# Optimization experiments

Measured on AMD Instinct MI355X. Metric: run time of the kernel, lower is better.

## Reference

```python
import jax, jax.numpy as jnp
import numpy as np

DIM = 128       # model dim d
NEXP = 64       # number of experts
K = 2           # top-k (hardcoded in the module)
B, S = 1, 1024  # batch, seq
HID = DIM * 4   # expert FFN hidden = 4*d


def _gelu(v):
    # torch F.gelu / nn.GELU default = exact erf form
    return jax.nn.gelu(v, approximate=False)


def setup_inputs() -> dict:
    key = jax.random.key(0)
    ks = jax.random.split(key, 8)
    sc = 0.02
    xav = (2.0 / (HID + DIM)) ** 0.5  # xavier_normal std for [4d, d]
    x = jax.random.normal(ks[0], (B, S, DIM), jnp.float32)
    # gate MLP: Linear(d,4d) -> GELU -> Linear(4d,4d) -> GELU -> Linear(4d,E) -> Sigmoid
    gw1 = jax.random.normal(ks[1], (DIM, HID), jnp.float32) * sc
    gb1 = jnp.zeros((HID,), jnp.float32)
    gw2 = jax.random.normal(ks[2], (HID, HID), jnp.float32) * sc
    gb2 = jnp.zeros((HID,), jnp.float32)
    gw3 = jax.random.normal(ks[3], (HID, NEXP), jnp.float32) * sc
    gb3 = jnp.zeros((NEXP,), jnp.float32)
    # expert banks (shapes fixed to the consistent 2-layer FFN reading)
    W1 = jax.random.normal(ks[4], (NEXP, HID, DIM), jnp.float32) * xav
    B1 = jnp.zeros((NEXP, HID), jnp.float32)
    W2 = jax.random.normal(ks[5], (NEXP, DIM, HID), jnp.float32) * xav
    B2 = jnp.zeros((NEXP, DIM), jnp.float32)
    return dict(x=x, gw1=gw1, gb1=gb1, gw2=gw2, gb2=gb2, gw3=gw3, gb3=gb3,
                W1=W1, B1=B1, W2=W2, B2=B2)


def reference(x, gw1, gb1, gw2, gb2, gw3, gb3, W1, B1, W2, B2):
    # gating network -> sigmoid scores over experts
    h = _gelu(x @ gw1 + gb1)
    h = _gelu(h @ gw2 + gb2)
    gate = jax.nn.sigmoid(h @ gw3 + gb3)                 # [B,S,E]
    values, idx = jax.lax.top_k(gate, K)                 # [B,S,K]
    values = values / jnp.sum(values, axis=-1, keepdims=True)
    # naive per-token gather of full expert weights (matches original access pattern)
    w1g = W1[idx]                                        # [B,S,K,HID,DIM]
    b1g = B1[idx]                                        # [B,S,K,HID]
    w2g = W2[idx]                                        # [B,S,K,DIM,HID]
    b2g = B2[idx]                                        # [B,S,K,DIM]
    t = _gelu(jnp.einsum('bskfd,bsd->bskf', w1g, x) + b1g)   # [B,S,K,HID]
    y = _gelu(jnp.einsum('bskdf,bskf->bskd', w2g, t) + b2g)  # [B,S,K,DIM]
    return jnp.sum(y * values[..., None], axis=-2)           # [B,S,DIM]
```

## Files before the change

kernel.cpp:

```cpp
#include <hip/hip_runtime.h>
#include <math.h>

#define NDIM 128
#define NHID 512
#define NEXPERT 64
#define NTOK 1024
#define NPAIR (NTOK * 2)

typedef __attribute__((ext_vector_type(8))) short short8_t;
typedef __attribute__((ext_vector_type(4))) float f32x4;

__device__ __forceinline__ float gelu_f(float v) {
    return 0.5f * v * (1.0f + erff(v * 0.7071067811865476f));
}
__device__ __forceinline__ unsigned short f2bf(float f) {
    union { float f; unsigned u; } v; v.f = f;
    unsigned r = v.u + 0x7FFFu + ((v.u >> 16) & 1u);
    return (unsigned short)(r >> 16);
}
__device__ __forceinline__ float bf2f(unsigned short h) {
    union { unsigned u; float f; } v; v.u = ((unsigned)h) << 16;
    return v.f;
}
__device__ __forceinline__ void split3(float f, short& ho, short& mo, short& lo) {
    const unsigned short h = f2bf(f);
    const float r1 = f - bf2f(h);
    const unsigned short m = f2bf(r1);
    const unsigned short l = f2bf(r1 - bf2f(m));
    ho = (short)h; mo = (short)m; lo = (short)l;
}

__global__ __launch_bounds__(256) void k_g1d2(
        const float* __restrict__ x, const float* __restrict__ gw1,
        const float* __restrict__ gw2, const float* __restrict__ gb1,
        unsigned short* __restrict__ G2h, unsigned short* __restrict__ G2m,
        unsigned short* __restrict__ G2l, unsigned short* __restrict__ Hh,
        unsigned short* __restrict__ Hm, unsigned short* __restrict__ Hl) {
    __shared__ __align__(16) char smem[58112];
    const int j = threadIdx.x;
    if (blockIdx.x >= 256) {
        float (*T)[65] = (float (*)[65])smem;
        const int u = blockIdx.x - 256;
        const int k0 = (u >> 3) * 64, n0 = (u & 7) * 64;
#pragma unroll
        for (int q = 0; q < 4; ++q) {
            const int idx = j + 256 * q;
            const int kr = idx >> 4, c4 = idx & 15;
            float4 v = *(const float4*)(gw2 + (size_t)(k0 + kr) * NHID + n0 + c4 * 4);
            T[kr][c4 * 4 + 0] = v.x; T[kr][c4 * 4 + 1] = v.y;
            T[kr][c4 * 4 + 2] = v.z; T[kr][c4 * 4 + 3] = v.w;
        }
        __syncthreads();
#pragma unroll
        for (int q = 0; q < 4; ++q) {
            const int idx = j + 256 * q;
            const int n = idx >> 4, k4 = idx & 15;
            short4 sh, sm, sl;
#pragma unroll
            for (int qq = 0; qq < 4; ++qq)
                split3(T[k4 * 4 + qq][n], (&sh.x)[qq], (&sm.x)[qq], (&sl.x)[qq]);
            const size_t o = (size_t)(n0 + n) * NHID + k0 + k4 * 4;
            *(short4*)(G2h + o) = sh;
            *(short4*)(G2m + o) = sm;
            *(short4*)(G2l + o) = sl;
        }
        return;
    }
    short (*Ahs)[32][72] = (short (*)[32][72])smem;
    short (*Bss)[64][72] = (short (*)[64][72])(smem + 13824);
    float (*T)[65] = (float (*)[65])(smem + 41472);
    const int u = blockIdx.x;
    const int m0 = (u >> 3) * 32, n0 = (u & 7) * 64;
    const int w = j >> 6, lane = j & 63;
    const int mt = w & 1, npair = w >> 1;
    const int lrow = lane & 15, lseg = lane >> 4;
    f32x4 acc[2];
    acc[0] = (f32x4){0.f, 0.f, 0.f, 0.f};
    acc[1] = (f32x4){0.f, 0.f, 0.f, 0.f};
    for (int kc = 0; kc < NDIM; kc += 64) {
        __syncthreads();
#pragma unroll
        for (int q = 0; q < 4; ++q) {
            const int idx = j + 256 * q;
            const int kr = idx >> 4, c4 = idx & 15;
            float4 v = *(const float4*)(gw1 + (size_t)(kc + kr) * NHID + n0 + c4 * 4);
            T[kr][c4 * 4 + 0] = v.x; T[kr][c4 * 4 + 1] = v.y;
            T[kr][c4 * 4 + 2] = v.z; T[kr][c4 * 4 + 3] = v.w;
        }
#pragma unroll
        for (int q = 0; q < 2; ++q) {
            const int idx = j + 256 * q;
            const int row = idx >> 4, c4 = idx & 15;
            float4 v = *(const float4*)(x + (size_t)(m0 + row) * NDIM + kc + c4 * 4);
            short4 sh, sm, sl;
#pragma unroll
            for (int qq = 0; qq < 4; ++qq)
                split3((&v.x)[qq], (&sh.x)[qq], (&sm.x)[qq], (&sl.x)[qq]);
            *(short4*)&Ahs[0][row][c4 * 4] = sh;
            *(short4*)&Ahs[1][row][c4 * 4] = sm;
            *(short4*)&Ahs[2][row][c4 * 4] = sl;
        }
        __syncthreads();
#pragma unroll
        for (int q = 0; q < 4; ++q) {
            const int idx = j + 256 * q;
            const int nn = idx >> 4, k4 = idx & 15;
            short4 sh, sm, sl;
#pragma unroll
            for (int qq = 0; qq < 4; ++qq)
                split3(T[k4 * 4 + qq][nn], (&sh.x)[qq], (&sm.x)[qq], (&sl.x)[qq]);
            *(short4*)&Bss[0][nn][k4 * 4] = sh;
            *(short4*)&Bss[1][nn][k4 * 4] = sm;
            *(short4*)&Bss[2][nn][k4 * 4] = sl;
        }
        __syncthreads();
#pragma unroll
        for (int ks = 0; ks < 2; ++ks) {
            const int ko = ks * 32 + lseg * 8;
            short8_t ah = *(short8_t*)&Ahs[0][mt * 16 + lrow][ko];
            short8_t am = *(short8_t*)&Ahs[1][mt * 16 + lrow][ko];
            short8_t al = *(short8_t*)&Ahs[2][mt * 16 + lrow][ko];
#pragma unroll
            for (int nt = 0; nt < 2; ++nt) {
                const int nr = (npair * 2 + nt) * 16 + lrow;
                short8_t bh = *(short8_t*)&Bss[0][nr][ko];
                short8_t bm = *(short8_t*)&Bss[1][nr][ko];
                short8_t bl = *(short8_t*)&Bss[2][nr][ko];
                acc[nt] = __builtin_amdgcn_mfma_f32_16x16x32_bf16(ah, bh, acc[nt], 0, 0, 0);
                acc[nt] = __builtin_amdgcn_mfma_f32_16x16x32_bf16(am, bh, acc[nt], 0, 0, 0);
                acc[nt] = __builtin_amdgcn_mfma_f32_16x16x32_bf16(ah, bm, acc[nt], 0, 0, 0);
                acc[nt] = __builtin_amdgcn_mfma_f32_16x16x32_bf16(al, bh, acc[nt], 0, 0, 0);
                acc[nt] = __builtin_amdgcn_mfma_f32_16x16x32_bf16(ah, bl, acc[nt], 0, 0, 0);
                acc[nt] = __builtin_amdgcn_mfma_f32_16x16x32_bf16(am, bm, acc[nt], 0, 0, 0);
            }
        }
    }
#pragma unroll
    for (int nt = 0; nt < 2; ++nt) {
        const int col = n0 + (npair * 2 + nt) * 16 + lrow;
        const float bb = gb1[col];
#pragma unroll
        for (int r = 0; r < 4; ++r) {
            const int row = m0 + mt * 16 + lseg * 4 + r;
            const float h = gelu_f(acc[nt][r] + bb);
            short hh, hm, hl;
            split3(h, hh, hm, hl);
            const size_t o = (size_t)row * NHID + col;
            Hh[o] = (unsigned short)hh; Hm[o] = (unsigned short)hm;
            Hl[o] = (unsigned short)hl;
        }
    }
}

__global__ __launch_bounds__(256) void k_gate2(
        const unsigned short* __restrict__ Ahp, const unsigned short* __restrict__ Amp,
        const unsigned short* __restrict__ Alp,
        const unsigned short* __restrict__ Bhp, const unsigned short* __restrict__ Bmp,
        const unsigned short* __restrict__ Blp,
        const float* __restrict__ gb2, float* __restrict__ h2) {
    __shared__ short Ahs[3][32][72];
    __shared__ short Bss[3][64][72];
    const int j = threadIdx.x;
    const int u = blockIdx.x;
    const int m0 = (u >> 3) * 32, n0 = (u & 7) * 64;
    const int w = j >> 6, lane = j & 63;
    const int mt = w & 1, npair = w >> 1;
    const int lrow = lane & 15, lseg = lane >> 4;
    const int K = NHID;
    f32x4 acc[2];
    acc[0] = (f32x4){0.f, 0.f, 0.f, 0.f};
    acc[1] = (f32x4){0.f, 0.f, 0.f, 0.f};
    for (int kc = 0; kc < K; kc += 64) {
        __syncthreads();
        {
            const int row = j >> 3, c8 = j & 7;
            const size_t o = (size_t)(m0 + row) * K + kc + c8 * 8;
            *(short8_t*)&Ahs[0][row][c8 * 8] = *(const short8_t*)(Ahp + o);
            *(short8_t*)&Ahs[1][row][c8 * 8] = *(const short8_t*)(Amp + o);
            *(short8_t*)&Ahs[2][row][c8 * 8] = *(const short8_t*)(Alp + o);
        }
#pragma unroll
        for (int q = 0; q < 2; ++q) {
            const int idx = j + 256 * q;
            const int nr = idx >> 3, c8 = idx & 7;
            const size_t o = (size_t)(n0 + nr) * K + kc + c8 * 8;
            *(short8_t*)&Bss[0][nr][c8 * 8] = *(const short8_t*)(Bhp + o);
            *(short8_t*)&Bss[1][nr][c8 * 8] = *(const short8_t*)(Bmp + o);
            *(short8_t*)&Bss[2][nr][c8 * 8] = *(const short8_t*)(Blp + o);
        }
        __syncthreads();
#pragma unroll
        for (int ks = 0; ks < 2; ++ks) {
            const int ko = ks * 32 + lseg * 8;
            short8_t ah = *(short8_t*)&Ahs[0][mt * 16 + lrow][ko];
            short8_t am = *(short8_t*)&Ahs[1][mt * 16 + lrow][ko];
            short8_t al = *(short8_t*)&Ahs[2][mt * 16 + lrow][ko];
#pragma unroll
            for (int nt = 0; nt < 2; ++nt) {
                const int nr = (npair * 2 + nt) * 16 + lrow;
                short8_t bh = *(short8_t*)&Bss[0][nr][ko];
                short8_t bm = *(short8_t*)&Bss[1][nr][ko];
                short8_t bl = *(short8_t*)&Bss[2][nr][ko];
                acc[nt] = __builtin_amdgcn_mfma_f32_16x16x32_bf16(ah, bh, acc[nt], 0, 0, 0);
                acc[nt] = __builtin_amdgcn_mfma_f32_16x16x32_bf16(am, bh, acc[nt], 0, 0, 0);
                acc[nt] = __builtin_amdgcn_mfma_f32_16x16x32_bf16(ah, bm, acc[nt], 0, 0, 0);
                acc[nt] = __builtin_amdgcn_mfma_f32_16x16x32_bf16(al, bh, acc[nt], 0, 0, 0);
                acc[nt] = __builtin_amdgcn_mfma_f32_16x16x32_bf16(ah, bl, acc[nt], 0, 0, 0);
                acc[nt] = __builtin_amdgcn_mfma_f32_16x16x32_bf16(am, bm, acc[nt], 0, 0, 0);
            }
        }
    }
#pragma unroll
    for (int nt = 0; nt < 2; ++nt) {
        const int col = n0 + (npair * 2 + nt) * 16 + lrow;
        const float bb = gb2[col];
#pragma unroll
        for (int r = 0; r < 4; ++r) {
            const int row = m0 + mt * 16 + lseg * 4 + r;
            h2[(size_t)row * NHID + col] = gelu_f(acc[nt][r] + bb);
        }
    }
}

__global__ __launch_bounds__(256) void k_gate3(
        const float* __restrict__ h2, const float* __restrict__ gw3,
        const float* __restrict__ gb3, int* __restrict__ eidx,
        float* __restrict__ wval) {
    __shared__ float hs[4][132];
    __shared__ float gs[128][72];
    const int j = threadIdx.x;
    const int lane = j & 63;
    const int w = j >> 6;
    const int t0 = blockIdx.x * 4;
    float acc = 0.f;
    for (int k0 = 0; k0 < NHID; k0 += 128) {
        __syncthreads();
        if (j < 128) {
            const int tok = j >> 5, c4 = j & 31;
            *(float4*)&hs[tok][c4 * 4] =
                *(const float4*)(h2 + (size_t)(t0 + tok) * NHID + k0 + c4 * 4);
        }
#pragma unroll
        for (int q = 0; q < 8; ++q) {
            const int idx = j + 256 * q;
            const int kk = idx >> 4, c4 = idx & 15;
            *(float4*)&gs[kk][c4 * 4] =
                *(const float4*)(gw3 + (size_t)(k0 + kk) * NEXPERT + c4 * 4);
        }
        __syncthreads();
        for (int kk = 0; kk < 128; ++kk) acc += hs[w][kk] * gs[kk][lane];
    }
    const float bias = gb3[lane];
    {
        const int t = t0 + w;
        float s = 1.f / (1.f + expf(-(acc + bias)));
        float v = s; int ix = lane;
#pragma unroll
        for (int off = 32; off >= 1; off >>= 1) {
            float ov = __shfl_xor(v, off);
            int oi = __shfl_xor(ix, off);
            if (ov > v || (ov == v && oi < ix)) { v = ov; ix = oi; }
        }
        const float v0 = v; const int i0 = ix;
        float v2 = (lane == i0) ? -1.f : s; int ix2 = lane;
#pragma unroll
        for (int off = 32; off >= 1; off >>= 1) {
            float ov = __shfl_xor(v2, off);
            int oi = __shfl_xor(ix2, off);
            if (ov > v2 || (ov == v2 && oi < ix2)) { v2 = ov; ix2 = oi; }
        }
        if (lane == 0) {
            float inv = 1.f / (v0 + v2);
            eidx[t * 2] = i0;  eidx[t * 2 + 1] = ix2;
            wval[t * 2] = v0 * inv;  wval[t * 2 + 1] = v2 * inv;
        }
    }
}

__device__ __forceinline__ int build_list(
        const int* __restrict__ eidx, int e, int lane, int w,
        int* lst, int* wtot) {
    unsigned long long msk[8];
    const int b0 = w * 512;
    int tot = 0;
#pragma unroll
    for (int c = 0; c < 8; ++c) {
        const int i = b0 + c * 64 + lane;
        msk[c] = __ballot(eidx[i] == e);
        tot += (int)__popcll(msk[c]);
    }
    if (lane == 0) wtot[w] = tot;
    __syncthreads();
    int woff = 0;
    for (int q = 0; q < w; ++q) woff += wtot[q];
    int run = 0;
#pragma unroll
    for (int c = 0; c < 8; ++c) {
        const int i = b0 + c * 64 + lane;
        if ((msk[c] >> lane) & 1ull)
            lst[woff + run + (int)__popcll(msk[c] & ((1ull << lane) - 1ull))] = i;
        run += (int)__popcll(msk[c]);
    }
    const int n = wtot[0] + wtot[1] + wtot[2] + wtot[3];
    __syncthreads();
    return n;
}

__global__ __launch_bounds__(256) void k_l1(
        const float* __restrict__ x, const float* __restrict__ W1,
        const float* __restrict__ B1, const int* __restrict__ eidx,
        unsigned short* __restrict__ tbuf) {
    __shared__ short As_[32 * 136];
    __shared__ short Bs_[64 * 136];
    __shared__ int prs[32];
    __shared__ int wtot[4];
    __shared__ int lst[NPAIR];
    const int j = threadIdx.x;
    const int lane = j & 63;
    const int w = j >> 6;
    const int e = blockIdx.x & 63;
    const int f0 = (blockIdx.x >> 6) * 64;
    char* Asc = (char*)As_;
    char* Bsc = (char*)Bs_;
    const int n = build_list(eidx, e, lane, w, lst, wtot);
    const float* W1e = W1 + (size_t)e * NHID * NDIM;
    for (int idx = j; idx < 2048; idx += 256) {
        const int f = idx >> 5, c4 = idx & 31;
        float4 v = *(const float4*)(W1e + (size_t)(f0 + f) * NDIM + c4 * 4);
        short4 s; s.x = (short)f2bf(v.x); s.y = (short)f2bf(v.y);
        s.z = (short)f2bf(v.z); s.w = (short)f2bf(v.w);
        *(short4*)(Bsc + f * 272 + c4 * 8) = s;
    }
    const float bbias = B1[e * NHID + f0 + w * 16 + (lane & 15)];
    for (int bt = 0; bt * 32 < n; ++bt) {
        __syncthreads();
        if (j < 32) prs[j] = (bt * 32 + j < n) ? lst[bt * 32 + j] : -1;
        __syncthreads();
        for (int idx = j; idx < 1024; idx += 256) {
            const int tok = idx >> 5, c4 = idx & 31;
            const int pr = prs[tok];
            float4 v = make_float4(0.f, 0.f, 0.f, 0.f);
            if (pr >= 0) v = ((const float4*)x)[(size_t)(pr >> 1) * 32 + c4];
            short4 s; s.x = (short)f2bf(v.x); s.y = (short)f2bf(v.y);
            s.z = (short)f2bf(v.z); s.w = (short)f2bf(v.w);
            *(short4*)(Asc + tok * 272 + c4 * 8) = s;
        }
        __syncthreads();
        f32x4 acc[2];
        acc[0] = (f32x4){0.f, 0.f, 0.f, 0.f};
        acc[1] = (f32x4){0.f, 0.f, 0.f, 0.f};
        const int acol = ((lane >> 4) << 4);
        const int brow = w * 16 + (lane & 15);
#pragma unroll
        for (int ks = 0; ks < 4; ++ks) {
            short8_t b = *(short8_t*)(Bsc + brow * 272 + ks * 64 + acol);
#pragma unroll
            for (int mt = 0; mt < 2; ++mt) {
                short8_t a = *(short8_t*)(Asc + (mt * 16 + (lane & 15)) * 272 + ks * 64 + acol);
                acc[mt] = __builtin_amdgcn_mfma_f32_16x16x32_bf16(a, b, acc[mt], 0, 0, 0);
            }
        }
        const int fcol = f0 + w * 16 + (lane & 15);
#pragma unroll
        for (int mt = 0; mt < 2; ++mt) {
#pragma unroll
            for (int r = 0; r < 4; ++r) {
                const int tok = mt * 16 + ((lane >> 4) << 2) + r;
                const int pr = prs[tok];
                if (pr >= 0)
                    tbuf[(size_t)pr * NHID + fcol] = f2bf(gelu_f(acc[mt][r] + bbias));
            }
        }
    }
}

__global__ __launch_bounds__(256) void k_l2(
        const float* __restrict__ W2, const int* __restrict__ eidx,
        const unsigned short* __restrict__ tbuf, float* __restrict__ pbuf) {
    __shared__ short As_[32 * 136];
    __shared__ short Bs_[64 * 136];
    __shared__ int prs[32];
    __shared__ int wtot[4];
    __shared__ int lst[NPAIR];
    const int j = threadIdx.x;
    const int lane = j & 63;
    const int w = j >> 6;
    const int e = blockIdx.x & 63;
    const int u = blockIdx.x >> 6;
    const int d0 = (u & 1) * 64;
    const int kz = u >> 1;
    const int k0 = kz * 128;
    char* Asc = (char*)As_;
    char* Bsc = (char*)Bs_;
    const int n = build_list(eidx, e, lane, w, lst, wtot);
    const float* W2e = W2 + (size_t)e * NDIM * NHID;
    for (int idx = j; idx < 2048; idx += 256) {
        const int d = idx >> 5, c4 = idx & 31;
        float4 v = *(const float4*)(W2e + (size_t)(d0 + d) * NHID + k0 + c4 * 4);
        short4 s; s.x = (short)f2bf(v.x); s.y = (short)f2bf(v.y);
        s.z = (short)f2bf(v.z); s.w = (short)f2bf(v.w);
        *(short4*)(Bsc + d * 272 + c4 * 8) = s;
    }
    float* pz = pbuf + (size_t)kz * NPAIR * NDIM;
    for (int bt = 0; bt * 32 < n; ++bt) {
        __syncthreads();
        if (j < 32) prs[j] = (bt * 32 + j < n) ? lst[bt * 32 + j] : -1;
        __syncthreads();
        for (int idx = j; idx < 512; idx += 256) {
            const int tok = idx >> 4, c8 = idx & 15;
            const int pr = prs[tok];
            short8_t v = (short8_t)(short)0;
            if (pr >= 0) v = *(const short8_t*)(tbuf + (size_t)pr * NHID + k0 + c8 * 8);
            *(short8_t*)(Asc + tok * 272 + c8 * 16) = v;
        }
        __syncthreads();
        f32x4 acc[2];
        acc[0] = (f32x4){0.f, 0.f, 0.f, 0.f};
        acc[1] = (f32x4){0.f, 0.f, 0.f, 0.f};
        const int acol = ((lane >> 4) << 4);
        const int brow = w * 16 + (lane & 15);
#pragma unroll
        for (int ks = 0; ks < 4; ++ks) {
            short8_t b = *(short8_t*)(Bsc + brow * 272 + ks * 64 + acol);
#pragma unroll
            for (int mt = 0; mt < 2; ++mt) {
                short8_t a = *(short8_t*)(Asc + (mt * 16 + (lane & 15)) * 272 + ks * 64 + acol);
                acc[mt] = __builtin_amdgcn_mfma_f32_16x16x32_bf16(a, b, acc[mt], 0, 0, 0);
            }
        }
        const int dcol = d0 + w * 16 + (lane & 15);
#pragma unroll
        for (int mt = 0; mt < 2; ++mt) {
#pragma unroll
            for (int r = 0; r < 4; ++r) {
                const int tok = mt * 16 + ((lane >> 4) << 2) + r;
                const int pr = prs[tok];
                if (pr >= 0) pz[(size_t)pr * NDIM + dcol] = acc[mt][r];
            }
        }
    }
}

__global__ __launch_bounds__(256) void k_combine(
        const float* __restrict__ pbuf, const float* __restrict__ wval,
        const int* __restrict__ eidx, const float* __restrict__ B2,
        float* __restrict__ out) {
    const int i = blockIdx.x * 256 + threadIdx.x;
    const int t = i >> 7, d = i & (NDIM - 1);
    const int KS = NPAIR * NDIM;
    float y[2];
#pragma unroll
    for (int k = 0; k < 2; ++k) {
        const int p = t * 2 + k;
        float s = pbuf[p * NDIM + d] + pbuf[KS + p * NDIM + d]
                + pbuf[2 * KS + p * NDIM + d] + pbuf[3 * KS + p * NDIM + d]
                + B2[eidx[p] * NDIM + d];
        y[k] = gelu_f(s);
    }
    out[i] = wval[t * 2] * y[0] + wval[t * 2 + 1] * y[1];
}

extern "C" void kernel_launch(void* const* d_in, const int* in_sizes, int n_in,
                              void* d_out, int out_size, void* d_ws, size_t ws_size,
                              hipStream_t stream) {
    const float* x   = (const float*)d_in[0];
    const float* gw1 = (const float*)d_in[1];
    const float* gb1 = (const float*)d_in[2];
    const float* gw2 = (const float*)d_in[3];
    const float* gb2 = (const float*)d_in[4];
    const float* gw3 = (const float*)d_in[5];
    const float* gb3 = (const float*)d_in[6];
    const float* W1  = (const float*)d_in[7];
    const float* B1  = (const float*)d_in[8];
    const float* W2  = (const float*)d_in[9];
    const float* B2  = (const float*)d_in[10];
    float* out = (float*)d_out;
    char* ws = (char*)d_ws;

    unsigned short* G2h = (unsigned short*)(ws);
    unsigned short* G2m = (unsigned short*)(ws + 524288);
    unsigned short* G2l = (unsigned short*)(ws + 1048576);
    unsigned short* Hh  = (unsigned short*)(ws + 1572864);
    unsigned short* Hm  = (unsigned short*)(ws + 2621440);
    unsigned short* Hl  = (unsigned short*)(ws + 3670016);
    float*          h2  = (float*)(ws + 4718592);
    unsigned short* tbuf = (unsigned short*)(ws);
    float*          pbuf = (float*)(ws + 2097152);
    int*   eidx = (int*)  (ws + 7340032);
    float* wval = (float*)(ws + 7340032 + 8192);

    k_g1d2<<<dim3(320), 256, 0, stream>>>(x, gw1, gw2, gb1, G2h, G2m, G2l, Hh, Hm, Hl);
    k_gate2<<<dim3(256), 256, 0, stream>>>(Hh, Hm, Hl, G2h, G2m, G2l, gb2, h2);
    k_gate3<<<dim3(256), 256, 0, stream>>>(h2, gw3, gb3, eidx, wval);
    k_l1<<<dim3(512), 256, 0, stream>>>(x, W1, B1, eidx, tbuf);
    k_l2<<<dim3(512), 256, 0, stream>>>(W2, eidx, tbuf, pbuf);
    k_combine<<<dim3(512), 256, 0, stream>>>(pbuf, wval, eidx, B2, out);
}
```

Measured before the change: 59.63 us.

## Fuse combine into k_l2 via last-arriving-block reduction with atomics

Removes the separate combine kernel. Each k_l2 block now bumps a per-(expert, d-half) arrival counter, and the last of the four K-split blocks sums the partials, adds bias, applies GELU and atomically adds the weighted result into the output. k_gate3 now zeroes the output and the counters beforehand. This saves one launch and the full pass over pbuf, at the cost of float atomics (non-deterministic summation order), fences, and serial tail work in the last block of each group.

```diff
diff --git a/kernel.cpp b/kernel.cpp
--- a/kernel.cpp
+++ b/kernel.cpp
@@ -225,13 +225,16 @@
 __global__ __launch_bounds__(256) void k_gate3(
         const float* __restrict__ h2, const float* __restrict__ gw3,
         const float* __restrict__ gb3, int* __restrict__ eidx,
-        float* __restrict__ wval) {
+        float* __restrict__ wval, float* __restrict__ out,
+        int* __restrict__ cnt2) {
     __shared__ float hs[4][132];
     __shared__ float gs[128][72];
     const int j = threadIdx.x;
     const int lane = j & 63;
     const int w = j >> 6;
     const int t0 = blockIdx.x * 4;
+    ((float2*)out)[blockIdx.x * 256 + j] = make_float2(0.f, 0.f);
+    if (blockIdx.x == 0 && j < NEXPERT * 2) cnt2[j] = 0;
     float acc = 0.f;
     for (int k0 = 0; k0 < NHID; k0 += 128) {
         __syncthreads();
@@ -375,13 +378,16 @@
 }
 
 __global__ __launch_bounds__(256) void k_l2(
-        const float* __restrict__ W2, const int* __restrict__ eidx,
-        const unsigned short* __restrict__ tbuf, float* __restrict__ pbuf) {
+        const float* __restrict__ W2, const float* __restrict__ B2,
+        const int* __restrict__ eidx, const float* __restrict__ wval,
+        const unsigned short* __restrict__ tbuf, float* __restrict__ pbuf,
+        int* __restrict__ cnt2, float* __restrict__ out) {
     __shared__ short As_[32 * 136];
     __shared__ short Bs_[64 * 136];
     __shared__ int prs[32];
     __shared__ int wtot[4];
     __shared__ int lst[NPAIR];
+    __shared__ int arrival;
     const int j = threadIdx.x;
     const int lane = j & 63;
     const int w = j >> 6;
@@ -439,25 +445,25 @@
             }
         }
     }
-}
-
-__global__ __launch_bounds__(256) void k_combine(
-        const float* __restrict__ pbuf, const float* __restrict__ wval,
-        const int* __restrict__ eidx, const float* __restrict__ B2,
-        float* __restrict__ out) {
-    const int i = blockIdx.x * 256 + threadIdx.x;
-    const int t = i >> 7, d = i & (NDIM - 1);
-    const int KS = NPAIR * NDIM;
-    float y[2];
-#pragma unroll
-    for (int k = 0; k < 2; ++k) {
-        const int p = t * 2 + k;
-        float s = pbuf[p * NDIM + d] + pbuf[KS + p * NDIM + d]
-                + pbuf[2 * KS + p * NDIM + d] + pbuf[3 * KS + p * NDIM + d]
-                + B2[eidx[p] * NDIM + d];
-        y[k] = gelu_f(s);
-    }
-    out[i] = wval[t * 2] * y[0] + wval[t * 2 + 1] * y[1];
+    __syncthreads();
+    if (j == 0) {
+        __threadfence();
+        arrival = atomicAdd(&cnt2[e * 2 + (d0 >> 6)], 1);
+    }
+    __syncthreads();
+    if (arrival == 3) {
+        __threadfence();
+        const int KS = NPAIR * NDIM;
+        for (int idx = j; idx < n * 64; idx += 256) {
+            const int tok = idx >> 6, dl = idx & 63;
+            const int pr = lst[tok];
+            const int dcol = d0 + dl;
+            const size_t off = (size_t)pr * NDIM + dcol;
+            float s = pbuf[off] + pbuf[KS + off] + pbuf[2 * KS + off]
+                    + pbuf[3 * KS + off] + B2[e * NDIM + dcol];
+            atomicAdd(&out[(size_t)(pr >> 1) * NDIM + dcol], wval[pr] * gelu_f(s));
+        }
+    }
 }
 
 extern "C" void kernel_launch(void* const* d_in, const int* in_sizes, int n_in,
@@ -488,11 +494,11 @@
     float*          pbuf = (float*)(ws + 2097152);
     int*   eidx = (int*)  (ws + 7340032);
     float* wval = (float*)(ws + 7340032 + 8192);
+    int*   cnt2 = (int*)  (ws + 7340032 + 16384);
 
     k_g1d2<<<dim3(320), 256, 0, stream>>>(x, gw1, gw2, gb1, G2h, G2m, G2l, Hh, Hm, Hl);
     k_gate2<<<dim3(256), 256, 0, stream>>>(Hh, Hm, Hl, G2h, G2m, G2l, gb2, h2);
-    k_gate3<<<dim3(256), 256, 0, stream>>>(h2, gw3, gb3, eidx, wval);
+    k_gate3<<<dim3(256), 256, 0, stream>>>(h2, gw3, gb3, eidx, wval, out, cnt2);
     k_l1<<<dim3(512), 256, 0, stream>>>(x, W1, B1, eidx, tbuf);
-    k_l2<<<dim3(512), 256, 0, stream>>>(W2, eidx, tbuf, pbuf);
-    k_combine<<<dim3(512), 256, 0, stream>>>(pbuf, wval, eidx, B2, out);
-}
+    k_l2<<<dim3(512), 256, 0, stream>>>(W2, B2, eidx, wval, tbuf, pbuf, cnt2, out);
+}
```

Result: slower. 90.18 us (+51.2%).
